# Optimization experiments

Hardware: AMD Instinct MI355X
Metric: run time of the kernel (lower is better)

Reference implementation:

```python
import jax, jax.numpy as jnp
import numpy as np

ALPHA = 0.2  # LeakyReLU negative slope
NEG_INF = -9e15


def setup_inputs() -> dict:
    key = jax.random.key(0)
    k1, k2, k3, k4, k5 = jax.random.split(key, 5)
    B, N, D = 4, 4096, 256
    feat = jax.random.normal(k1, (B, N, D), dtype=jnp.float32)
    adj = jax.random.randint(k2, (B, N, N), 0, 2, dtype=jnp.int32)
    W = jax.random.normal(k3, (D, D), dtype=jnp.float32) * (1.414 / np.sqrt(D))
    a_1 = jax.random.normal(k4, (D, 1), dtype=jnp.float32) * 0.1
    a_2 = jax.random.normal(k5, (D, 1), dtype=jnp.float32) * 0.1
    return {"feat": feat, "adj": adj, "W": W, "a_1": a_1, "a_2": a_2}


def reference(feat, adj, W, a_1, a_2):
    # h: [B, N, D]
    h = jnp.matmul(feat, W)
    Ax = jnp.matmul(h, a_1)  # [B, N, 1]
    Ay = jnp.matmul(h, a_2)  # [B, N, 1]
    # logits[b, i, j] = Ax[b, j] + Ay[b, i]
    logits = jnp.swapaxes(Ax, 1, 2) + Ay  # [B, N, N]
    e = jax.nn.leaky_relu(logits, negative_slope=ALPHA)
    e = jnp.where(adj > 0, e, jnp.float32(NEG_INF))
    attention = jax.nn.softmax(e, axis=-1)  # dropout p=0.0 -> identity
    h_prime = jnp.matmul(attention, feat)  # [B, N, in_features]
    h_out = jnp.matmul(h_prime, W)  # [B, N, out_features]
    return jax.nn.elu(h_out)
```

## Files before the change

kernel.cpp:

```cpp
#include <hip/hip_runtime.h>

typedef __attribute__((ext_vector_type(8))) short short8;
typedef __attribute__((ext_vector_type(4))) float f32x4;
typedef __attribute__((ext_vector_type(4))) int i32x4;
typedef __attribute__((ext_vector_type(2))) unsigned u32x2;

#define LOG2E 1.44269504f

__device__ __forceinline__ short f2bf(float f) {
  unsigned u = __builtin_bit_cast(unsigned, f);
  u += 0x7fffu + ((u >> 16) & 1u);
  return (short)(u >> 16);
}

__global__ __launch_bounds__(256) void gat_pro(
    const float* __restrict__ feat, const float* __restrict__ W,
    const float* __restrict__ a1, const float* __restrict__ a2,
    short* __restrict__ featB, short* __restrict__ WB,
    float* __restrict__ AxL, float* __restrict__ AyL) {
  __shared__ __align__(16) float a1f[256], a2f[256];
  __shared__ __align__(16) float w1f[256], w2f[256];
  __shared__ __align__(16) float tile[32][260];
  const int tid = threadIdx.x;
  const int f = blockIdx.x, b = blockIdx.y;

  a1f[tid] = a1[tid];
  a2f[tid] = a2[tid];
  __syncthreads();

  {
    float s1 = 0.f, s2 = 0.f;
    const float4* wr = (const float4*)(W + (size_t)tid * 256);
    for (int d0 = 0; d0 < 64; ++d0) {
      float4 v = wr[d0];
      s1 += v.x * a1f[d0 * 4] + v.y * a1f[d0 * 4 + 1] + v.z * a1f[d0 * 4 + 2] + v.w * a1f[d0 * 4 + 3];
      s2 += v.x * a2f[d0 * 4] + v.y * a2f[d0 * 4 + 1] + v.z * a2f[d0 * 4 + 2] + v.w * a2f[d0 * 4 + 3];
    }
    w1f[tid] = s1;
    w2f[tid] = s2;
  }
  __syncthreads();

  {
    const int r = tid >> 3, g8 = tid & 7;
    const float* frow = feat + ((size_t)(b * 4096 + f * 32 + r)) * 256;
    float s1 = 0.f, s2 = 0.f;
#pragma unroll
    for (int k = 0; k < 8; ++k) {
      const int c4 = g8 + 8 * k;
      float4 v = *(const float4*)(frow + c4 * 4);
      float4 u1 = *(const float4*)&w1f[c4 * 4];
      float4 u2 = *(const float4*)&w2f[c4 * 4];
      s1 += v.x * u1.x + v.y * u1.y + v.z * u1.z + v.w * u1.w;
      s2 += v.x * u2.x + v.y * u2.y + v.z * u2.z + v.w * u2.w;
      *(float4*)&tile[r][c4 * 4] = v;
    }
#pragma unroll
    for (int off = 4; off >= 1; off >>= 1) {
      s1 += __shfl_xor(s1, off);
      s2 += __shfl_xor(s2, off);
    }
    if (g8 == 0) {
      AxL[b * 4096 + f * 32 + r] = s1 * LOG2E;
      AyL[b * 4096 + f * 32 + r] = s2 * LOG2E;
    }
  }
  __syncthreads();

  {
    const int g = tid >> 4, l15 = tid & 15;
    short* d = featB + (((size_t)((b * 128 + f) * 16 + g)) * 64) * 8;
#pragma unroll
    for (int q = 0; q < 4; ++q) {
      short8 v;
#pragma unroll
      for (int j8 = 0; j8 < 8; ++j8) v[j8] = f2bf(tile[q * 8 + j8][g * 16 + l15]);
      *(short8*)(d + (q * 16 + l15) * 8) = v;
    }
  }

  if (b == 0 && f < 8) {
    const int g = tid >> 4, l15 = tid & 15;
    const float* s = W + ((size_t)f * 32) * 256 + g * 16 + l15;
    short* d = WB + (((size_t)(f * 16 + g)) * 64) * 8;
#pragma unroll
    for (int q = 0; q < 4; ++q) {
      short8 v;
#pragma unroll
      for (int j8 = 0; j8 < 8; ++j8) v[j8] = f2bf(s[(q * 8 + j8) * 256]);
      *(short8*)(d + (q * 16 + l15) * 8) = v;
    }
  }
}

__global__ void gat_max(const float* __restrict__ AxL, float* __restrict__ MbL) {
  __shared__ float red[256];
  const int b = blockIdx.x, tid = threadIdx.x;
  float m = -3.4e38f;
  for (int i = tid; i < 4096; i += 256) m = fmaxf(m, AxL[b * 4096 + i]);
  red[tid] = m;
  __syncthreads();
  for (int s = 128; s > 0; s >>= 1) {
    if (tid < s) red[tid] = fmaxf(red[tid], red[tid + s]);
    __syncthreads();
  }
  if (tid == 0) MbL[b] = red[0];
}

__global__ __launch_bounds__(512, 4) void gat_attn(
    const short* __restrict__ featB,
    const int* __restrict__ adj,
    const float* __restrict__ AxL, const float* __restrict__ AyL,
    const float* __restrict__ MbL,
    const short* __restrict__ WB,
    float* __restrict__ out)
{
  __shared__ short smem[16896];

  const int tid = threadIdx.x;
  const int blk = blockIdx.x;
  const int x = blk & 7;
  const int b = x >> 1;
  const int it = ((blk >> 3) << 1) | (x & 1);
  const int i0 = it << 5;
  const int scoff = (blk >> 3) & 15;

  const int lane = tid & 63;
  const int aw = tid >> 6;

  float aLk[4], ddk[4];
#pragma unroll
  for (int k = 0; k < 4; ++k) {
    float ayL = AyL[b * 4096 + i0 + aw * 4 + k];
    float sL = ayL + MbL[b];
    float mrL = fmaxf(sL, 0.2f * sL);
    aLk[k] = ayL - mrL;
    ddk[k] = -0.8f * mrL;
  }
  const int* adjr = adj + ((size_t)(b * 4096 + i0 + aw * 4)) * 4096 + lane * 4;
  const float4* axp = (const float4*)(AxL + b * 4096) + lane;

  const int w = aw;
  const int rowg = (w & 1) << 4;
  const int cgrp = (w >> 1) << 2;
  const int l15 = lane & 15;
  const int q = lane >> 4;

  f32x4 acc[4], lac;
  lac = (f32x4){0.f, 0.f, 0.f, 0.f};
#pragma unroll
  for (int j = 0; j < 4; ++j) acc[j] = (f32x4){0.f, 0.f, 0.f, 0.f};

  short8 ones;
#pragma unroll
  for (int j = 0; j < 8; ++j) ones[j] = (short)0x3F80;

  const short* fbb = featB + (size_t)b * 128 * 16 * 64 * 8 + lane * 8;

  i32x4 adv[4];
  float4 axv;
  {
    const int w0 = scoff;
    axv = axp[w0 * 64];
#pragma unroll
    for (int k = 0; k < 4; ++k)
      adv[k] = __builtin_nontemporal_load((const i32x4*)(adjr) + k * 1024 + w0 * 64);
  }

  for (int sc = 0; sc < 16; ++sc) {
    const int wsc = (scoff + sc) & 15;
    const int pb = (sc & 1) * 8448;
    {
      const float* af = (const float*)&axv;
#pragma unroll
      for (int k = 0; k < 4; ++k) {
        unsigned pr[4];
#pragma unroll
        for (int u = 0; u < 4; ++u) {
          float v = af[u] + aLk[k];
          float uu = fmaxf(v, fmaf(0.2f, v, ddk[k]));
          unsigned ub = adv[k][u] > 0 ? __builtin_bit_cast(unsigned, uu) : 0xFF800000u;
          float p = __builtin_amdgcn_exp2f(__builtin_bit_cast(float, ub));
          pr[u] = __builtin_bit_cast(unsigned, p) + 0x8000u;
        }
        u32x2 pw;
        pw[0] = __builtin_amdgcn_perm(pr[1], pr[0], 0x07060302u);
        pw[1] = __builtin_amdgcn_perm(pr[3], pr[2], 0x07060302u);
        *(u32x2*)(smem + pb + (aw * 4 + k) * 264 + lane * 4) = pw;
      }
    }
    __syncthreads();

    if (sc < 15) {
      const int wn = (scoff + sc + 1) & 15;
      axv = axp[wn * 64];
#pragma unroll
      for (int k = 0; k < 4; ++k)
        adv[k] = __builtin_nontemporal_load((const i32x4*)(adjr) + k * 1024 + wn * 64);
    }

#pragma unroll
    for (int h = 0; h < 8; ++h) {
      const int f = wsc * 8 + h;
      const short* fb = fbb + (((size_t)f * 16 + cgrp) << 9);
      short8 a = *(const short8*)(smem + pb + (rowg + l15) * 264 + h * 32 + q * 8);
      lac = __builtin_amdgcn_mfma_f32_16x16x32_bf16(a, ones, lac, 0, 0, 0);
#pragma unroll
      for (int ct = 0; ct < 4; ++ct) {
        short8 bf = *(const short8*)(fb + (ct << 9));
        acc[ct] = __builtin_amdgcn_mfma_f32_16x16x32_bf16(a, bf, acc[ct], 0, 0, 0);
      }
    }
  }

  float linv[4];
#pragma unroll
  for (int reg = 0; reg < 4; ++reg) {
    float l = lac[reg];
    linv[reg] = l > 0.f ? 1.f / l : 0.f;
  }

  __syncthreads();
  short* hbuf = smem;
#pragma unroll
  for (int reg = 0; reg < 4; ++reg) {
    const int lr = rowg + q * 4 + reg;
#pragma unroll
    for (int ct = 0; ct < 4; ++ct)
      hbuf[lr * 264 + cgrp * 16 + ct * 16 + l15] = f2bf(acc[ct][reg] * linv[reg]);
  }
  __syncthreads();

  f32x4 ac2[4];
#pragma unroll
  for (int j = 0; j < 4; ++j) ac2[j] = (f32x4){0.f, 0.f, 0.f, 0.f};

  const short* wbb = WB + lane * 8;
#pragma unroll
  for (int f = 0; f < 8; ++f) {
    short8 a = *(const short8*)&hbuf[(rowg + l15) * 264 + f * 32 + q * 8];
    const short* wb = wbb + (((size_t)f * 16 + cgrp) << 9);
#pragma unroll
    for (int ct = 0; ct < 4; ++ct) {
      short8 bf = *(const short8*)(wb + (ct << 9));
      ac2[ct] = __builtin_amdgcn_mfma_f32_16x16x32_bf16(a, bf, ac2[ct], 0, 0, 0);
    }
  }

#pragma unroll
  for (int reg = 0; reg < 4; ++reg) {
    const int row = i0 + rowg + q * 4 + reg;
    float* orow = out + ((size_t)(b * 4096 + row)) * 256 + cgrp * 16 + l15;
#pragma unroll
    for (int ct = 0; ct < 4; ++ct) {
      float v = ac2[ct][reg];
      float o = v > 0.f ? v : (__builtin_amdgcn_exp2f(v * LOG2E) - 1.f);
      __builtin_nontemporal_store(o, orow + ct * 16);
    }
  }
}

extern "C" void kernel_launch(void* const* d_in, const int* in_sizes, int n_in,
                              void* d_out, int out_size, void* d_ws, size_t ws_size,
                              hipStream_t stream) {
  (void)in_sizes; (void)n_in; (void)out_size; (void)ws_size;
  const float* feat = (const float*)d_in[0];
  const int* adj = (const int*)d_in[1];
  const float* W = (const float*)d_in[2];
  const float* a1 = (const float*)d_in[3];
  const float* a2 = (const float*)d_in[4];
  float* out = (float*)d_out;

  char* ws = (char*)d_ws;
  short* featB   = (short*)ws;
  short* WB      = (short*)(ws + 8388608);
  float* AxL     = (float*)(ws + 8519680);
  float* AyL     = (float*)(ws + 8585216);
  float* MbL     = (float*)(ws + 8650752);
  (void)ws_size;

  hipLaunchKernelGGL(gat_pro, dim3(128, 4), dim3(256), 0, stream, feat, W, a1, a2, featB, WB, AxL, AyL);
  hipLaunchKernelGGL(gat_max, dim3(4), dim3(256), 0, stream, AxL, MbL);
  hipLaunchKernelGGL(gat_attn, dim3(512), dim3(512), 0, stream, featB, adj, AxL, AyL, MbL, WB, out);
}
```

Before: 436.7 us.

## Double rows per attention block and fuse per-batch max into attention kernel

Each attention block now processes 64 query rows instead of 32, so every feature tile loaded from global memory is reused by two MFMA row groups. The grid halves to 256 blocks and LDS doubles. The separate max-reduction kernel is removed and each block recomputes the per-batch max of Ax itself, saving a launch at the cost of redundant reads. Risks include lower occupancy (launch bounds 2), higher register pressure, and fewer blocks than ideal to fill the CUs.

```diff
diff --git a/kernel.cpp b/kernel.cpp
--- a/kernel.cpp
+++ b/kernel.cpp
@@ -93,63 +93,61 @@
   }
 }
 
-__global__ void gat_max(const float* __restrict__ AxL, float* __restrict__ MbL) {
-  __shared__ float red[256];
-  const int b = blockIdx.x, tid = threadIdx.x;
-  float m = -3.4e38f;
-  for (int i = tid; i < 4096; i += 256) m = fmaxf(m, AxL[b * 4096 + i]);
-  red[tid] = m;
-  __syncthreads();
-  for (int s = 128; s > 0; s >>= 1) {
-    if (tid < s) red[tid] = fmaxf(red[tid], red[tid + s]);
-    __syncthreads();
-  }
-  if (tid == 0) MbL[b] = red[0];
-}
-
-__global__ __launch_bounds__(512, 4) void gat_attn(
+__global__ __launch_bounds__(512, 2) void gat_attn(
     const short* __restrict__ featB,
     const int* __restrict__ adj,
     const float* __restrict__ AxL, const float* __restrict__ AyL,
-    const float* __restrict__ MbL,
     const short* __restrict__ WB,
     float* __restrict__ out)
 {
-  __shared__ short smem[16896];
+  __shared__ short smem[33792];
+  __shared__ float mred[8];
 
   const int tid = threadIdx.x;
   const int blk = blockIdx.x;
   const int x = blk & 7;
   const int b = x >> 1;
   const int it = ((blk >> 3) << 1) | (x & 1);
-  const int i0 = it << 5;
+  const int i0 = it << 6;
   const int scoff = (blk >> 3) & 15;
 
   const int lane = tid & 63;
   const int aw = tid >> 6;
 
-  float aLk[4], ddk[4];
-#pragma unroll
-  for (int k = 0; k < 4; ++k) {
-    float ayL = AyL[b * 4096 + i0 + aw * 4 + k];
-    float sL = ayL + MbL[b];
+  const float* axb = AxL + b * 4096;
+  float mx = -3.4e38f;
+  for (int i = tid; i < 4096; i += 512) mx = fmaxf(mx, axb[i]);
+#pragma unroll
+  for (int off = 32; off >= 1; off >>= 1) mx = fmaxf(mx, __shfl_xor(mx, off));
+  if (lane == 0) mred[aw] = mx;
+  __syncthreads();
+  const float MbLb = fmaxf(fmaxf(fmaxf(mred[0], mred[1]), fmaxf(mred[2], mred[3])),
+                           fmaxf(fmaxf(mred[4], mred[5]), fmaxf(mred[6], mred[7])));
+
+  float aLk[8], ddk[8];
+#pragma unroll
+  for (int k = 0; k < 8; ++k) {
+    float ayL = AyL[b * 4096 + i0 + aw * 8 + k];
+    float sL = ayL + MbLb;
     float mrL = fmaxf(sL, 0.2f * sL);
     aLk[k] = ayL - mrL;
     ddk[k] = -0.8f * mrL;
   }
-  const int* adjr = adj + ((size_t)(b * 4096 + i0 + aw * 4)) * 4096 + lane * 4;
+  const int* adjr = adj + ((size_t)(b * 4096 + i0 + aw * 8)) * 4096 + lane * 4;
   const float4* axp = (const float4*)(AxL + b * 4096) + lane;
 
-  const int w = aw;
-  const int rowg = (w & 1) << 4;
-  const int cgrp = (w >> 1) << 2;
+  const int rowg = (aw & 1) << 4;
+  const int cgrp = (aw >> 1) << 2;
   const int l15 = lane & 15;
   const int q = lane >> 4;
 
-  f32x4 acc[4], lac;
-  lac = (f32x4){0.f, 0.f, 0.f, 0.f};
-#pragma unroll
-  for (int j = 0; j < 4; ++j) acc[j] = (f32x4){0.f, 0.f, 0.f, 0.f};
+  f32x4 acc[2][4], lac[2];
+#pragma unroll
+  for (int r = 0; r < 2; ++r) {
+    lac[r] = (f32x4){0.f, 0.f, 0.f, 0.f};
+#pragma unroll
+    for (int j = 0; j < 4; ++j) acc[r][j] = (f32x4){0.f, 0.f, 0.f, 0.f};
+  }
 
   short8 ones;
 #pragma unroll
@@ -157,23 +155,23 @@
 
   const short* fbb = featB + (size_t)b * 128 * 16 * 64 * 8 + lane * 8;
 
-  i32x4 adv[4];
+  i32x4 adv[8];
   float4 axv;
   {
     const int w0 = scoff;
     axv = axp[w0 * 64];
 #pragma unroll
-    for (int k = 0; k < 4; ++k)
-      adv[k] = __builtin_nontemporal_load((const i32x4*)(adjr) + k * 1024 + w0 * 64);
+    for (int k = 0; k < 8; ++k)
+      adv[k] = __builtin_nontemporal_load((const i32x4*)(adjr) + (size_t)k * 1024 + w0 * 64);
   }
 
   for (int sc = 0; sc < 16; ++sc) {
     const int wsc = (scoff + sc) & 15;
-    const int pb = (sc & 1) * 8448;
+    const int pb = (sc & 1) * 16896;
     {
       const float* af = (const float*)&axv;
 #pragma unroll
-      for (int k = 0; k < 4; ++k) {
+      for (int k = 0; k < 8; ++k) {
         unsigned pr[4];
 #pragma unroll
         for (int u = 0; u < 4; ++u) {
@@ -186,7 +184,7 @@
         u32x2 pw;
         pw[0] = __builtin_amdgcn_perm(pr[1], pr[0], 0x07060302u);
         pw[1] = __builtin_amdgcn_perm(pr[3], pr[2], 0x07060302u);
-        *(u32x2*)(smem + pb + (aw * 4 + k) * 264 + lane * 4) = pw;
+        *(u32x2*)(smem + pb + (aw * 8 + k) * 264 + lane * 4) = pw;
       }
     }
     __syncthreads();
@@ -195,69 +193,82 @@
       const int wn = (scoff + sc + 1) & 15;
       axv = axp[wn * 64];
 #pragma unroll
-      for (int k = 0; k < 4; ++k)
-        adv[k] = __builtin_nontemporal_load((const i32x4*)(adjr) + k * 1024 + wn * 64);
+      for (int k = 0; k < 8; ++k)
+        adv[k] = __builtin_nontemporal_load((const i32x4*)(adjr) + (size_t)k * 1024 + wn * 64);
     }
 
 #pragma unroll
     for (int h = 0; h < 8; ++h) {
       const int f = wsc * 8 + h;
       const short* fb = fbb + (((size_t)f * 16 + cgrp) << 9);
-      short8 a = *(const short8*)(smem + pb + (rowg + l15) * 264 + h * 32 + q * 8);
-      lac = __builtin_amdgcn_mfma_f32_16x16x32_bf16(a, ones, lac, 0, 0, 0);
+      short8 a0 = *(const short8*)(smem + pb + (rowg + l15) * 264 + h * 32 + q * 8);
+      short8 a1 = *(const short8*)(smem + pb + (rowg + 32 + l15) * 264 + h * 32 + q * 8);
+      lac[0] = __builtin_amdgcn_mfma_f32_16x16x32_bf16(a0, ones, lac[0], 0, 0, 0);
+      lac[1] = __builtin_amdgcn_mfma_f32_16x16x32_bf16(a1, ones, lac[1], 0, 0, 0);
 #pragma unroll
       for (int ct = 0; ct < 4; ++ct) {
         short8 bf = *(const short8*)(fb + (ct << 9));
-        acc[ct] = __builtin_amdgcn_mfma_f32_16x16x32_bf16(a, bf, acc[ct], 0, 0, 0);
+        acc[0][ct] = __builtin_amdgcn_mfma_f32_16x16x32_bf16(a0, bf, acc[0][ct], 0, 0, 0);
+        acc[1][ct] = __builtin_amdgcn_mfma_f32_16x16x32_bf16(a1, bf, acc[1][ct], 0, 0, 0);
       }
     }
   }
 
-  float linv[4];
-#pragma unroll
-  for (int reg = 0; reg < 4; ++reg) {
-    float l = lac[reg];
-    linv[reg] = l > 0.f ? 1.f / l : 0.f;
-  }
+  float linv[2][4];
+#pragma unroll
+  for (int r = 0; r < 2; ++r)
+#pragma unroll
+    for (int reg = 0; reg < 4; ++reg) {
+      float l = lac[r][reg];
+      linv[r][reg] = l > 0.f ? 1.f / l : 0.f;
+    }
 
   __syncthreads();
   short* hbuf = smem;
 #pragma unroll
-  for (int reg = 0; reg < 4; ++reg) {
-    const int lr = rowg + q * 4 + reg;
-#pragma unroll
-    for (int ct = 0; ct < 4; ++ct)
-      hbuf[lr * 264 + cgrp * 16 + ct * 16 + l15] = f2bf(acc[ct][reg] * linv[reg]);
-  }
-  __syncthreads();
-
-  f32x4 ac2[4];
-#pragma unroll
-  for (int j = 0; j < 4; ++j) ac2[j] = (f32x4){0.f, 0.f, 0.f, 0.f};
+  for (int r = 0; r < 2; ++r)
+#pragma unroll
+    for (int reg = 0; reg < 4; ++reg) {
+      const int lr = rowg + r * 32 + q * 4 + reg;
+#pragma unroll
+      for (int ct = 0; ct < 4; ++ct)
+        hbuf[lr * 264 + cgrp * 16 + ct * 16 + l15] = f2bf(acc[r][ct][reg] * linv[r][reg]);
+    }
+  __syncthreads();
+
+  f32x4 ac2[2][4];
+#pragma unroll
+  for (int r = 0; r < 2; ++r)
+#pragma unroll
+    for (int j = 0; j < 4; ++j) ac2[r][j] = (f32x4){0.f, 0.f, 0.f, 0.f};
 
   const short* wbb = WB + lane * 8;
 #pragma unroll
   for (int f = 0; f < 8; ++f) {
-    short8 a = *(const short8*)&hbuf[(rowg + l15) * 264 + f * 32 + q * 8];
+    short8 a0 = *(const short8*)&hbuf[(rowg + l15) * 264 + f * 32 + q * 8];
+    short8 a1 = *(const short8*)&hbuf[(rowg + 32 + l15) * 264 + f * 32 + q * 8];
     const short* wb = wbb + (((size_t)f * 16 + cgrp) << 9);
 #pragma unroll
     for (int ct = 0; ct < 4; ++ct) {
       short8 bf = *(const short8*)(wb + (ct << 9));
-      ac2[ct] = __builtin_amdgcn_mfma_f32_16x16x32_bf16(a, bf, ac2[ct], 0, 0, 0);
-    }
-  }
-
-#pragma unroll
-  for (int reg = 0; reg < 4; ++reg) {
-    const int row = i0 + rowg + q * 4 + reg;
-    float* orow = out + ((size_t)(b * 4096 + row)) * 256 + cgrp * 16 + l15;
-#pragma unroll
-    for (int ct = 0; ct < 4; ++ct) {
-      float v = ac2[ct][reg];
-      float o = v > 0.f ? v : (__builtin_amdgcn_exp2f(v * LOG2E) - 1.f);
-      __builtin_nontemporal_store(o, orow + ct * 16);
-    }
-  }
+      ac2[0][ct] = __builtin_amdgcn_mfma_f32_16x16x32_bf16(a0, bf, ac2[0][ct], 0, 0, 0);
+      ac2[1][ct] = __builtin_amdgcn_mfma_f32_16x16x32_bf16(a1, bf, ac2[1][ct], 0, 0, 0);
+    }
+  }
+
+#pragma unroll
+  for (int r = 0; r < 2; ++r)
+#pragma unroll
+    for (int reg = 0; reg < 4; ++reg) {
+      const int row = i0 + rowg + r * 32 + q * 4 + reg;
+      float* orow = out + ((size_t)(b * 4096 + row)) * 256 + cgrp * 16 + l15;
+#pragma unroll
+      for (int ct = 0; ct < 4; ++ct) {
+        float v = ac2[r][ct][reg];
+        float o = v > 0.f ? v : (__builtin_amdgcn_exp2f(v * LOG2E) - 1.f);
+        __builtin_nontemporal_store(o, orow + ct * 16);
+      }
+    }
 }
 
 extern "C" void kernel_launch(void* const* d_in, const int* in_sizes, int n_in,
@@ -276,10 +287,7 @@
   short* WB      = (short*)(ws + 8388608);
   float* AxL     = (float*)(ws + 8519680);
   float* AyL     = (float*)(ws + 8585216);
-  float* MbL     = (float*)(ws + 8650752);
-  (void)ws_size;
 
   hipLaunchKernelGGL(gat_pro, dim3(128, 4), dim3(256), 0, stream, feat, W, a1, a2, featB, WB, AxL, AyL);
-  hipLaunchKernelGGL(gat_max, dim3(4), dim3(256), 0, stream, AxL, MbL);
-  hipLaunchKernelGGL(gat_attn, dim3(512), dim3(512), 0, stream, featB, adj, AxL, AyL, MbL, WB, out);
-}
+  hipLaunchKernelGGL(gat_attn, dim3(256), dim3(512), 0, stream, featB, adj, AxL, AyL, WB, out);
+}
```

Result: no change. 429.1 us (-1.7%).
